# Kernel tuning notes

Hardware: AMD Instinct MI355X
Metric: run time of the kernel (lower is better)

The kernel has to match this reference:

```python
import jax, jax.numpy as jnp
import numpy as np

N_NODES = 20000
N_EDGES = 320000
N_GRAPHS = 512
N_FEAT = 29
DIMS = [N_FEAT, 1024, 512, 256, 512, 1024]
EPS = 1e-5


def setup_inputs() -> dict:
    key = jax.random.key(0)
    ks = jax.random.split(key, 32)
    inp = {}
    inp["x"] = jax.random.normal(ks[0], (N_NODES, N_FEAT), dtype=jnp.float32)
    inp["edge_index"] = jax.random.randint(ks[1], (2, N_EDGES), 0, N_NODES, dtype=jnp.int64)
    inp["batch"] = jnp.sort(jax.random.randint(ks[2], (N_NODES,), 0, N_GRAPHS, dtype=jnp.int64))
    # 5 GCNConv layers: weight [in, out] + bias, plus BN gamma/beta
    for i in range(5):
        din, dout = DIMS[i], DIMS[i + 1]
        inp[f"W{i+1}"] = jax.random.normal(ks[3 + i], (din, dout), dtype=jnp.float32) * (1.0 / np.sqrt(din))
        inp[f"b{i+1}"] = jnp.zeros((dout,), dtype=jnp.float32)
        inp[f"g{i+1}"] = jnp.ones((dout,), dtype=jnp.float32)
        inp[f"be{i+1}"] = jnp.zeros((dout,), dtype=jnp.float32)
    # attention gate Linear(1024, 1)
    inp["Wg"] = jax.random.normal(ks[10], (1024, 1), dtype=jnp.float32) * 0.03
    inp["bg"] = jnp.zeros((1,), dtype=jnp.float32)
    # MLP head
    inp["Wf2"] = jax.random.normal(ks[11], (1024, 128), dtype=jnp.float32) * 0.03
    inp["bf2"] = jnp.zeros((128,), dtype=jnp.float32)
    inp["Wf3"] = jax.random.normal(ks[12], (128, 16), dtype=jnp.float32) * 0.25
    inp["bf3"] = jnp.zeros((16,), dtype=jnp.float32)
    inp["Wf4"] = jax.random.normal(ks[13], (16, 1), dtype=jnp.float32) * 0.25
    inp["bf4"] = jnp.zeros((1,), dtype=jnp.float32)
    return inp


def _gcn_conv(x, row, col, W, b):
    # PyG GCNConv: linear transform, then D^{-1/2}(A+I)D^{-1/2} aggregation, then bias.
    n = x.shape[0]
    xw = x @ W  # [N, dout]
    deg = jax.ops.segment_sum(jnp.ones_like(col, dtype=xw.dtype), col, num_segments=n)
    dinv = jnp.where(deg > 0, jax.lax.rsqrt(deg), 0.0)
    norm = dinv[row] * dinv[col]  # [E+N]
    out = jax.ops.segment_sum(xw[row] * norm[:, None], col, num_segments=n)
    return out + b


def _bn_train(x, gamma, beta):
    m = jnp.mean(x, axis=0)
    v = jnp.var(x, axis=0)  # biased, matches torch training normalization
    return gamma * (x - m) * jax.lax.rsqrt(v + EPS) + beta


def _global_attention(x, batch, Wg, bg, n_graphs):
    gate = (x @ Wg + bg)[:, 0]  # [N]
    gmax = jax.ops.segment_max(gate, batch, num_segments=n_graphs)
    e = jnp.exp(gate - gmax[batch])
    s = jax.ops.segment_sum(e, batch, num_segments=n_graphs)
    alpha = e / s[batch]
    return jax.ops.segment_sum(alpha[:, None] * x, batch, num_segments=n_graphs)


def reference(x, edge_index, batch,
              W1, b1, g1, be1, W2, b2, g2, be2, W3, b3, g3, be3,
              W4, b4, g4, be4, W5, b5, g5, be5,
              Wg, bg, Wf2, bf2, Wf3, bf3, Wf4, bf4):
    n = x.shape[0]
    sl = jnp.arange(n, dtype=edge_index.dtype)
    row = jnp.concatenate([edge_index[0], sl])  # with self-loops
    col = jnp.concatenate([edge_index[1], sl])
    h = x
    params = [(W1, b1, g1, be1), (W2, b2, g2, be2), (W3, b3, g3, be3),
              (W4, b4, g4, be4), (W5, b5, g5, be5)]
    for (W, b, g, be) in params:
        h = jax.nn.relu(_gcn_conv(h, row, col, W, b))
        h = _bn_train(h, g, be)
    p = _global_attention(h, batch, Wg, bg, N_GRAPHS)  # [G, 1024]
    p = jax.nn.relu(p @ Wf2 + bf2)
    p = jax.nn.relu(p @ Wf3 + bf3)
    return p @ Wf4 + bf4  # [G, 1]
```

## Files before the change

### kernel.cpp

```cpp
#include <hip/hip_runtime.h>

#define EPS_BN 1e-5f

constexpr int NN   = 20000;
constexpr int NE   = 320000;
constexpr int NTOT = NE + NN;
constexpr int NG   = 512;
constexpr int MPAD = 20480;
constexpr int NBLK = 79;

typedef _Float16 half8  __attribute__((ext_vector_type(8)));
typedef _Float16 half2v __attribute__((ext_vector_type(2)));
typedef float floatx4   __attribute__((ext_vector_type(4)));

__global__ void k_deg(const int* __restrict__ col, int* __restrict__ deg,
                      const int* __restrict__ batch, int* __restrict__ gcnt) {
  int e = blockIdx.x * blockDim.x + threadIdx.x;
  if (e >= NTOT) return;
  int c = (e < NE) ? col[e] : (e - NE);
  atomicAdd(&deg[c], 1);
  if (e < NN) atomicAdd(&gcnt[batch[e]], 1);
}

__global__ __launch_bounds__(256) void k_pre1(const int* __restrict__ deg,
                                              float* __restrict__ dinvv,
                                              int* __restrict__ psum) {
  __shared__ int ws[4];
  int t = threadIdx.x, lane = t & 63, wv = t >> 6;
  int idx = blockIdx.x * 256 + t;
  int d = (idx < NN) ? deg[idx] : 0;
  if (idx < NN) dinvv[idx] = rsqrtf((float)d);
  int s = d;
  for (int o = 1; o < 64; o <<= 1) { int u = __shfl_up(s, o, 64); if (lane >= o) s += u; }
  if (lane == 63) ws[wv] = s;
  __syncthreads();
  if (t == 0) psum[blockIdx.x] = ws[0] + ws[1] + ws[2] + ws[3];
}

__global__ __launch_bounds__(256) void k_pre2(const int* __restrict__ psum,
                                              int* __restrict__ pbase,
                                              const int* __restrict__ gcnt,
                                              int* __restrict__ goff) {
  __shared__ int ws[8];
  int t = threadIdx.x, lane = t & 63, wv = t >> 6;
  int v = (t < NBLK) ? psum[t] : 0;
  int inc = v;
  for (int o = 1; o < 64; o <<= 1) { int u = __shfl_up(inc, o, 64); if (lane >= o) inc += u; }
  if (lane == 63) ws[wv] = inc;
  __syncthreads();
  int base = 0;
  for (int w = 0; w < wv; ++w) base += ws[w];
  int excl = base + inc - v;
  if (t < NBLK) pbase[t] = excl;
  if (t == NBLK - 1) pbase[NBLK] = excl + v;
  __syncthreads();
  int a0 = gcnt[2 * t], a1 = gcnt[2 * t + 1];
  int p = a0 + a1;
  int incp = p;
  for (int o = 1; o < 64; o <<= 1) { int u = __shfl_up(incp, o, 64); if (lane >= o) incp += u; }
  if (lane == 63) ws[4 + wv] = incp;
  __syncthreads();
  int gb = 0;
  for (int w = 0; w < wv; ++w) gb += ws[4 + w];
  int exclp = gb + incp - p;
  goff[2 * t]     = exclp;
  goff[2 * t + 1] = exclp + a0;
  if (t == 255) goff[NG] = exclp + p;
}

__global__ __launch_bounds__(256) void k_pre3(const int* __restrict__ deg,
                                              const int* __restrict__ pbase,
                                              int* __restrict__ indptr,
                                              int* __restrict__ cursor) {
  __shared__ int ws[4];
  int t = threadIdx.x, lane = t & 63, wv = t >> 6;
  int idx = blockIdx.x * 256 + t;
  int d = (idx < NN) ? deg[idx] : 0;
  int inc = d;
  for (int o = 1; o < 64; o <<= 1) { int u = __shfl_up(inc, o, 64); if (lane >= o) inc += u; }
  if (lane == 63) ws[wv] = inc;
  __syncthreads();
  int base = pbase[blockIdx.x];
  for (int w = 0; w < wv; ++w) base += ws[w];
  int excl = base + inc - d;
  if (idx < NN) { indptr[idx] = excl; cursor[idx] = excl; }
  if (idx == NN - 1) indptr[NN] = excl + d;
}

__global__ void k_fill(const int* __restrict__ row, const int* __restrict__ col,
                       const float* __restrict__ dinv, int* __restrict__ cursor,
                       int2* __restrict__ csw, float* __restrict__ rsum) {
  int e = blockIdx.x * blockDim.x + threadIdx.x;
  if (e >= NTOT) return;
  int r, c;
  if (e < NE) { r = row[e]; c = col[e]; } else { r = c = e - NE; }
  float wv = dinv[r] * dinv[c];
  int pos = atomicAdd(&cursor[c], 1);
  int2 m; m.x = r; m.y = __builtin_bit_cast(int, wv);
  csw[pos] = m;
  atomicAdd(&rsum[c], wv);
}

__device__ __forceinline__ size_t fragoff(int n, int k, int kb) {
  return ((size_t)(n >> 4) * kb + (k >> 5)) * 512 + ((k >> 3) & 3) * 128 + (n & 15) * 8;
}

__global__ void k_wconv3(const float* __restrict__ W0, const float* __restrict__ W3,
                         const float* __restrict__ W4,
                         _Float16* __restrict__ T0, _Float16* __restrict__ T3,
                         _Float16* __restrict__ T4) {
  int c = blockIdx.x * blockDim.x + threadIdx.x;
  _Float16 ov[8];
  if (c < 4096) {
    int n = c >> 2, k = (c & 3) * 8;
    #pragma unroll
    for (int i = 0; i < 8; ++i)
      ov[i] = (_Float16)((k + i < 29) ? W0[(size_t)(k + i) * 1024 + n] : 0.f);
    *(uint4*)&T0[fragoff(n, k, 1)] = *(const uint4*)ov;
  } else if (c < 4096 + 16384) {
    int c2 = c - 4096;
    int n = c2 >> 5, k = (c2 & 31) * 8;
    #pragma unroll
    for (int i = 0; i < 8; ++i)
      ov[i] = (_Float16)W3[(size_t)(k + i) * 512 + n];
    *(uint4*)&T3[fragoff(n, k, 8)] = *(const uint4*)ov;
  } else if (c < 4096 + 16384 + 65536) {
    int c3 = c - 20480;
    int n = c3 >> 6, k = (c3 & 63) * 8;
    #pragma unroll
    for (int i = 0; i < 8; ++i)
      ov[i] = (_Float16)W4[(size_t)(k + i) * 1024 + n];
    *(uint4*)&T4[fragoff(n, k, 16)] = *(const uint4*)ov;
  }
}

__global__ __launch_bounds__(256) void k_wfold(const float* __restrict__ W, int K, int N,
                                               const float* __restrict__ sums,
                                               const float* __restrict__ gamma,
                                               const float* __restrict__ beta,
                                               _Float16* __restrict__ T,
                                               float* __restrict__ c) {
  __shared__ float red[256];
  int n = blockIdx.x, tid = threadIdx.x;
  int kb = K >> 5;
  const float inv_n = 1.f / NN;
  float csum = 0.f;
  for (int kc = tid; kc < (K >> 3); kc += 256) {
    int k = kc * 8;
    _Float16 ov[8];
    #pragma unroll
    for (int i = 0; i < 8; ++i) {
      int ki = k + i;
      float mean = sums[ki] * inv_n;
      float var  = sums[K + ki] * inv_n - mean * mean;
      float sc   = gamma[ki] * rsqrtf(var + EPS_BN);
      float sh   = beta[ki] - mean * sc;
      float wv   = W[(size_t)ki * N + n];
      ov[i] = (_Float16)(sc * wv);
      csum += sh * wv;
    }
    *(uint4*)&T[fragoff(n, k, kb)] = *(const uint4*)ov;
  }
  red[tid] = csum;
  __syncthreads();
  for (int o = 128; o > 0; o >>= 1) {
    if (tid < o) red[tid] += red[tid + o];
    __syncthreads();
  }
  if (tid == 0) c[n] = red[0];
}

#define AGG_CH 128
__global__ __launch_bounds__(128) void k_agg29(
    const float* __restrict__ X,
    const int* __restrict__ indptr, const int2* __restrict__ csw,
    _Float16* __restrict__ Y) {
  __shared__ int   s_src[AGG_CH];
  __shared__ float s_w[AGG_CH];
  __shared__ float red[128];
  int node = blockIdx.x;
  int tid  = threadIdx.x;
  int sub  = tid / 29;
  int feat = tid - sub * 29;
  bool act = tid < 116;
  int beg = indptr[node], end = indptr[node + 1];
  float acc = 0.f;
  for (int e0 = beg; e0 < end; e0 += AGG_CH) {
    int c = min(AGG_CH, end - e0);
    if (tid < c) {
      int2 m = csw[e0 + tid];
      s_src[tid] = m.x;
      s_w[tid]   = __builtin_bit_cast(float, m.y);
    }
    __syncthreads();
    if (act) {
      for (int j = 0; j < c; j += 4) {
        int jj = j + sub;
        if (jj < c) acc += s_w[jj] * X[(size_t)s_src[jj] * 29 + feat];
      }
    }
    __syncthreads();
  }
  red[tid] = acc;
  __syncthreads();
  if (tid < 32) {
    float v = 0.f;
    if (tid < 29) v = red[tid] + red[29 + tid] + red[58 + tid] + red[87 + tid];
    size_t fb = (size_t)(node >> 4) * 512 + (size_t)(tid >> 3) * 128 + (node & 15) * 8 + (tid & 7);
    Y[fb] = (_Float16)v;
  }
}

template<int MODE>
__global__ __launch_bounds__(256) void k_aggv(
    const _Float16* __restrict__ X,
    _Float16* __restrict__ Yf, _Float16* __restrict__ Yrow,
    const int* __restrict__ indptr, const int2* __restrict__ csw,
    const float* __restrict__ rowsum,
    const float* __restrict__ p0, const float* __restrict__ p1,
    const float* __restrict__ p2)
{
  constexpr int F = 512;
  int wave = threadIdx.x >> 6;
  int lane = threadIdx.x & 63;
  int node = blockIdx.x * 4 + wave;
  int beg = indptr[node], end = indptr[node + 1];
  float acc[8];
  #pragma unroll
  for (int i = 0; i < 8; ++i) acc[i] = 0.f;
  const unsigned* Xl = (const unsigned*)X + lane * 4;

  auto body = [&](int e) {
    int2 m = csw[e];
    float we = __builtin_bit_cast(float, m.y);
    uint4 d = *(const uint4*)(Xl + (size_t)m.x * (F / 2));
    unsigned uu[4] = {d.x, d.y, d.z, d.w};
    #pragma unroll
    for (int i = 0; i < 4; ++i) {
      half2v h = __builtin_bit_cast(half2v, uu[i]);
      acc[2 * i]     = fmaf(we, (float)h[0], acc[2 * i]);
      acc[2 * i + 1] = fmaf(we, (float)h[1], acc[2 * i + 1]);
    }
  };
  int e = beg;
  for (; e + 8 <= end; e += 8) {
    body(e); body(e + 1); body(e + 2); body(e + 3);
    body(e + 4); body(e + 5); body(e + 6); body(e + 7);
  }
  for (; e < end; ++e) body(e);

  float s_n = rowsum[node];
  _Float16 outv[8];
  #pragma unroll
  for (int i = 0; i < 8; ++i) {
    int f = lane * 8 + i;
    float v;
    if constexpr (MODE == 0) {
      v = fmaxf(acc[i] + s_n * p0[f] + p1[f], 0.f);
    } else {
      const float inv_n = 1.f / NN;
      float mean = p0[f] * inv_n;
      float var  = p0[F + f] * inv_n - mean * mean;
      float sc   = p1[f] * rsqrtf(var + EPS_BN);
      float sh   = p2[f] - mean * sc;
      v = sc * acc[i] + s_n * sh;
    }
    outv[i] = (_Float16)v;
  }
  if (Yf) {
    size_t fb = (size_t)(node >> 4) * (16 * 512) + lane * 128 + (node & 15) * 8;
    *(uint4*)(Yf + fb) = *(const uint4*)outv;
  }
  if (Yrow) {
    *(uint4*)(Yrow + (size_t)node * F + lane * 8) = *(const uint4*)outv;
  }
}

template<int MODE>
__global__ __launch_bounds__(256) void k_aggp(
    const _Float16* __restrict__ X,
    _Float16* __restrict__ Yf, _Float16* __restrict__ Yrow,
    const int* __restrict__ indptr, const int2* __restrict__ csw,
    const float* __restrict__ rowsum,
    const float* __restrict__ p0, const float* __restrict__ p1,
    const float* __restrict__ p2)
{
  constexpr int F = 256;
  int wave = threadIdx.x >> 6;
  int lane = threadIdx.x & 63;
  int half = lane >> 5;
  int l32  = lane & 31;
  int node = blockIdx.x * 8 + wave * 2 + half;
  int beg = indptr[node], end = indptr[node + 1];
  int len = end - beg;
  int len0 = __shfl(len, 0, 64);
  int len1 = __shfl(len, 32, 64);
  int maxlen = max(len0, len1);

  float acc[8];
  #pragma unroll
  for (int i = 0; i < 8; ++i) acc[i] = 0.f;
  const unsigned* Xl = (const unsigned*)X + l32 * 4;

  auto body = [&](int t) {
    int e = beg + min(t, len - 1);
    int2 m = csw[e];
    float we = (t < len) ? __builtin_bit_cast(float, m.y) : 0.f;
    uint4 d = *(const uint4*)(Xl + (size_t)m.x * (F / 2));
    unsigned uu[4] = {d.x, d.y, d.z, d.w};
    #pragma unroll
    for (int i = 0; i < 4; ++i) {
      half2v h = __builtin_bit_cast(half2v, uu[i]);
      acc[2 * i]     = fmaf(we, (float)h[0], acc[2 * i]);
      acc[2 * i + 1] = fmaf(we, (float)h[1], acc[2 * i + 1]);
    }
  };
  int t = 0;
  for (; t + 4 <= maxlen; t += 4) { body(t); body(t + 1); body(t + 2); body(t + 3); }
  for (; t < maxlen; ++t) body(t);

  float s_n = rowsum[node];
  _Float16 outv[8];
  #pragma unroll
  for (int i = 0; i < 8; ++i) {
    int f = l32 * 8 + i;
    float v;
    if constexpr (MODE == 0) {
      v = fmaxf(acc[i] + s_n * p0[f] + p1[f], 0.f);
    } else {
      const float inv_n = 1.f / NN;
      float mean = p0[f] * inv_n;
      float var  = p0[F + f] * inv_n - mean * mean;
      float sc   = p1[f] * rsqrtf(var + EPS_BN);
      float sh   = p2[f] - mean * sc;
      v = sc * acc[i] + s_n * sh;
    }
    outv[i] = (_Float16)v;
  }
  if (Yf) {
    size_t fb = (size_t)(node >> 4) * (8 * 512) + l32 * 128 + (node & 15) * 8;
    *(uint4*)(Yf + fb) = *(const uint4*)outv;
  }
  if (Yrow) {
    *(uint4*)(Yrow + (size_t)node * F + l32 * 8) = *(const uint4*)outv;
  }
}

template<int K, int FRAGOUT>
__global__ __launch_bounds__(256) void k_gemmf(
    const _Float16* __restrict__ Af, const _Float16* __restrict__ Bf,
    const float* __restrict__ bias,
    _Float16* __restrict__ Ch,
    _Float16* __restrict__ Cf,
    float* __restrict__ stats,
    int N, int do_relu, int nbx)
{
  __shared__ __align__(16) _Float16 cs[128 * 136];
  __shared__ float sred[256];

  const int tid  = threadIdx.x;
  const int wave = tid >> 6;
  const int lane = tid & 63;

  int lin = blockIdx.x;
  int xcd = lin & 7, seq = lin >> 3;
  int bx = seq % nbx, grp = seq / nbx;
  int by = xcd + 8 * grp;
  const int row0 = by * 128;
  const int col0 = bx * 128;

  const int q  = lane >> 4;
  const int mm = lane & 15;
  const int wm = wave >> 1;
  const int wn = wave & 1;

  sred[tid] = 0.f;

  constexpr int KB = K / 32;
  const _Float16* pa[4];
  const _Float16* pb[4];
  #pragma unroll
  for (int i = 0; i < 4; ++i)
    pa[i] = Af + (size_t)((row0 >> 4) + wm * 4 + i) * (KB * 512) + lane * 8;
  #pragma unroll
  for (int j = 0; j < 4; ++j)
    pb[j] = Bf + (size_t)((col0 >> 4) + wn * 4 + j) * (KB * 512) + lane * 8;

  floatx4 acc[4][4];
  #pragma unroll
  for (int i = 0; i < 4; ++i)
    #pragma unroll
    for (int j = 0; j < 4; ++j) acc[i][j] = floatx4{0.f, 0.f, 0.f, 0.f};

  half8 av[4], bv[4];
  #pragma unroll
  for (int i = 0; i < 4; ++i) { av[i] = *(const half8*)pa[i]; pa[i] += 512; }
  #pragma unroll
  for (int j = 0; j < 4; ++j) { bv[j] = *(const half8*)pb[j]; pb[j] += 512; }

  #pragma unroll 2
  for (int s = 0; s < KB; ++s) {
    half8 nav[4], nbv[4];
    if (s + 1 < KB) {
      #pragma unroll
      for (int i = 0; i < 4; ++i) { nav[i] = *(const half8*)pa[i]; pa[i] += 512; }
      #pragma unroll
      for (int j = 0; j < 4; ++j) { nbv[j] = *(const half8*)pb[j]; pb[j] += 512; }
    }
    #pragma unroll
    for (int j = 0; j < 4; ++j)
      #pragma unroll
      for (int i = 0; i < 4; ++i)
        acc[i][j] = __builtin_amdgcn_mfma_f32_16x16x32_f16(av[i], bv[j], acc[i][j], 0, 0, 0);
    if (s + 1 < KB) {
      #pragma unroll
      for (int i = 0; i < 4; ++i) av[i] = nav[i];
      #pragma unroll
      for (int j = 0; j < 4; ++j) bv[j] = nbv[j];
    }
  }

  __syncthreads();

  float sloc[4]  = {0.f, 0.f, 0.f, 0.f};
  float s2loc[4] = {0.f, 0.f, 0.f, 0.f};
  #pragma unroll
  for (int j = 0; j < 4; ++j) {
    int cl = wn * 64 + j * 16 + mm;
    float bvv = bias ? bias[col0 + cl] : 0.f;
    #pragma unroll
    for (int i = 0; i < 4; ++i) {
      #pragma unroll
      for (int r = 0; r < 4; ++r) {
        int rl = wm * 64 + i * 16 + q * 4 + r;
        float v = acc[i][j][r] + bvv;
        if (do_relu) v = fmaxf(v, 0.f);
        cs[rl * 136 + cl] = (_Float16)v;
        if (row0 + rl < NN) { sloc[j] += v; s2loc[j] += v * v; }
      }
    }
  }

  if (stats) {
    #pragma unroll
    for (int j = 0; j < 4; ++j) {
      float a = sloc[j], b2 = s2loc[j];
      a  += __shfl_xor(a, 16, 64);  a  += __shfl_xor(a, 32, 64);
      b2 += __shfl_xor(b2, 16, 64); b2 += __shfl_xor(b2, 32, 64);
      if (q == 0) {
        int cl = wn * 64 + j * 16 + mm;
        atomicAdd(&sred[cl], a);
        atomicAdd(&sred[128 + cl], b2);
      }
    }
  }
  __syncthreads();

  if (FRAGOUT) {
    int mlo = tid & 15, sub = (tid >> 4) & 3, kcr = (tid >> 6) & 3;
    int kbN = N >> 5;
    #pragma unroll
    for (int pass = 0; pass < 8; ++pass) {
      int m = pass * 16 + mlo;
      int kl = kcr * 32 + sub * 8;
      uint4 d = *(const uint4*)&cs[m * 136 + kl];
      size_t fa = ((size_t)((row0 >> 4) + pass) * kbN + (col0 >> 5) + kcr) * 512
                + sub * 128 + mlo * 8;
      *(uint4*)&Cf[fa] = d;
    }
  } else {
    #pragma unroll
    for (int pass = 0; pass < 8; ++pass) {
      int cidx = tid + pass * 256;
      int r = cidx >> 4, kc = cidx & 15;
      int rr = row0 + r;
      if (rr < NN) {
        uint4 d = *(const uint4*)&cs[r * 136 + kc * 8];
        *(uint4*)&Ch[(size_t)rr * N + col0 + kc * 8] = d;
      }
    }
  }

  if (stats && tid < 128) {
    atomicAdd(&stats[col0 + tid], sred[tid]);
    atomicAdd(&stats[N + col0 + tid], sred[128 + tid]);
  }
}

template<int F>
__global__ __launch_bounds__(256) void k_statsf(const _Float16* __restrict__ Xf,
                                                float* __restrict__ sums) {
  constexpr int KB = F / 32;
  constexpr int NT = NN / 16;
  int wid  = (blockIdx.x * 256 + threadIdx.x) >> 6;
  int lane = threadIdx.x & 63;
  int nw   = (gridDim.x * 256) >> 6;
  int kidx = wid % KB;
  int ng0  = wid / KB;
  int step = nw / KB;
  int sub = lane >> 4, n16 = lane & 15;

  float s[8], s2[8];
  #pragma unroll
  for (int i = 0; i < 8; ++i) { s[i] = 0.f; s2[i] = 0.f; }

  for (int ng = ng0; ng < NT; ng += step) {
    const _Float16* p = Xf + ((size_t)ng * KB + kidx) * 512 + lane * 8;
    uint4 d = *(const uint4*)p;
    unsigned uu[4] = {d.x, d.y, d.z, d.w};
    #pragma unroll
    for (int i = 0; i < 4; ++i) {
      half2v h = __builtin_bit_cast(half2v, uu[i]);
      float v0 = (float)h[0], v1 = (float)h[1];
      s[2 * i]      += v0;  s2[2 * i]     += v0 * v0;
      s[2 * i + 1]  += v1;  s2[2 * i + 1] += v1 * v1;
    }
  }
  #pragma unroll
  for (int o = 1; o < 16; o <<= 1) {
    #pragma unroll
    for (int i = 0; i < 8; ++i) {
      s[i]  += __shfl_xor(s[i],  o, 64);
      s2[i] += __shfl_xor(s2[i], o, 64);
    }
  }
  if (n16 == 0) {
    int f = kidx * 32 + sub * 8;
    #pragma unroll
    for (int i = 0; i < 8; ++i) {
      atomicAdd(&sums[f + i], s[i]);
      atomicAdd(&sums[F + f + i], s2[i]);
    }
  }
}

__global__ __launch_bounds__(256) void k_stats16(const _Float16* __restrict__ X, int F,
                                                 float* __restrict__ sums) {
  int tid = threadIdx.x;
  int npf = F >> 8;
  float s[2] = {0.f, 0.f}, s2[2] = {0.f, 0.f};
  for (int r = blockIdx.x; r < NN; r += gridDim.x) {
    #pragma unroll
    for (int i = 0; i < 2; ++i) {
      if (i < npf) {
        float v = (float)X[(size_t)r * F + tid + i * 256];
        s[i] += v; s2[i] += v * v;
      }
    }
  }
  #pragma unroll
  for (int i = 0; i < 2; ++i) {
    if (i < npf) {
      atomicAdd(&sums[tid + i * 256], s[i]);
      atomicAdd(&sums[F + tid + i * 256], s2[i]);
    }
  }
}

__global__ __launch_bounds__(256) void k_gfold(const float* __restrict__ sums,
                                               const float* __restrict__ g5,
                                               const float* __restrict__ be5,
                                               const float* __restrict__ Wg,
                                               const float* __restrict__ bg,
                                               float* __restrict__ wgf,
                                               float* __restrict__ cg) {
  __shared__ float red[256];
  int tid = threadIdx.x;
  const float inv_n = 1.f / NN;
  float t = 0.f;
  #pragma unroll
  for (int i = 0; i < 4; ++i) {
    int f = i * 256 + tid;
    float mean = sums[f] * inv_n;
    float var  = sums[1024 + f] * inv_n - mean * mean;
    float sc   = g5[f] * rsqrtf(var + EPS_BN);
    float sh   = be5[f] - mean * sc;
    float wv   = Wg[f];
    wgf[f] = sc * wv;
    t += sh * wv;
  }
  red[tid] = t;
  __syncthreads();
  for (int o = 128; o > 0; o >>= 1) {
    if (tid < o) red[tid] += red[tid + o];
    __syncthreads();
  }
  if (tid == 0) cg[0] = red[0] + bg[0];
}

__global__ __launch_bounds__(256) void k_gate3(const _Float16* __restrict__ X,
                                               const float* __restrict__ wgf,
                                               const float* __restrict__ cg,
                                               float* __restrict__ gate) {
  int wave = threadIdx.x >> 6, lane = threadIdx.x & 63;
  int node = blockIdx.x * 4 + wave;
  const _Float16* xp = X + (size_t)node * 1024 + lane * 16;
  uint4 d0 = *(const uint4*)xp;
  uint4 d1 = *(const uint4*)(xp + 8);
  const float4* wp = (const float4*)(wgf + lane * 16);
  float4 w0 = wp[0], w1 = wp[1], w2 = wp[2], w3 = wp[3];
  float wv[16] = {w0.x, w0.y, w0.z, w0.w, w1.x, w1.y, w1.z, w1.w,
                  w2.x, w2.y, w2.z, w2.w, w3.x, w3.y, w3.z, w3.w};
  unsigned uu[8] = {d0.x, d0.y, d0.z, d0.w, d1.x, d1.y, d1.z, d1.w};
  float s = 0.f;
  #pragma unroll
  for (int i = 0; i < 8; ++i) {
    half2v h = __builtin_bit_cast(half2v, uu[i]);
    s = fmaf((float)h[0], wv[2 * i],     s);
    s = fmaf((float)h[1], wv[2 * i + 1], s);
  }
  #pragma unroll
  for (int o = 1; o < 64; o <<= 1) s += __shfl_xor(s, o, 64);
  if (lane == 0) gate[node] = s + cg[0];
}

__global__ __launch_bounds__(256) void k_poolhead(
    const _Float16* __restrict__ X, const float* __restrict__ gate,
    const int* __restrict__ goff,
    const float* __restrict__ sums, const float* __restrict__ g5,
    const float* __restrict__ be5,
    const float* __restrict__ Wf2, const float* __restrict__ bf2,
    const float* __restrict__ Wf3, const float* __restrict__ bf3,
    const float* __restrict__ Wf4, const float* __restrict__ bf4,
    float* __restrict__ out)
{
  __shared__ float red[256];
  __shared__ float sp[1024];
  __shared__ float sp2[128];
  __shared__ float sp3[16];
  int g = blockIdx.x, tid = threadIdx.x;
  int beg = goff[g], end = goff[g + 1];
  bool nonempty = end > beg;

  float m = -3.4e38f;
  for (int n = beg + tid; n < end; n += 256) m = fmaxf(m, gate[n]);
  red[tid] = m;
  __syncthreads();
  for (int o = 128; o > 0; o >>= 1) {
    if (tid < o) red[tid] = fmaxf(red[tid], red[tid + o]);
    __syncthreads();
  }
  m = red[0];
  __syncthreads();
  float s = 0.f;
  for (int n = beg + tid; n < end; n += 256) s += expf(gate[n] - m);
  red[tid] = s;
  __syncthreads();
  for (int o = 128; o > 0; o >>= 1) {
    if (tid < o) red[tid] += red[tid + o];
    __syncthreads();
  }
  float inv = nonempty ? (1.f / red[0]) : 0.f;

  int f = tid * 4;
  const float inv_n = 1.f / NN;
  float acc[4] = {0.f, 0.f, 0.f, 0.f};
  if (nonempty) {
    const _Float16* Xf = X + f;
    int n = beg;
    for (; n + 4 <= end; n += 4) {
      float a0 = expf(gate[n]     - m);
      float a1 = expf(gate[n + 1] - m);
      float a2 = expf(gate[n + 2] - m);
      float a3 = expf(gate[n + 3] - m);
      uint2 u0 = *(const uint2*)(Xf + (size_t)(n)     * 1024);
      uint2 u1 = *(const uint2*)(Xf + (size_t)(n + 1) * 1024);
      uint2 u2 = *(const uint2*)(Xf + (size_t)(n + 2) * 1024);
      uint2 u3 = *(const uint2*)(Xf + (size_t)(n + 3) * 1024);
      half2v p00 = __builtin_bit_cast(half2v, u0.x), p01 = __builtin_bit_cast(half2v, u0.y);
      half2v p10 = __builtin_bit_cast(half2v, u1.x), p11 = __builtin_bit_cast(half2v, u1.y);
      half2v p20 = __builtin_bit_cast(half2v, u2.x), p21 = __builtin_bit_cast(half2v, u2.y);
      half2v p30 = __builtin_bit_cast(half2v, u3.x), p31 = __builtin_bit_cast(half2v, u3.y);
      acc[0] += a0 * (float)p00[0] + a1 * (float)p10[0] + a2 * (float)p20[0] + a3 * (float)p30[0];
      acc[1] += a0 * (float)p00[1] + a1 * (float)p10[1] + a2 * (float)p20[1] + a3 * (float)p30[1];
      acc[2] += a0 * (float)p01[0] + a1 * (float)p11[0] + a2 * (float)p21[0] + a3 * (float)p31[0];
      acc[3] += a0 * (float)p01[1] + a1 * (float)p11[1] + a2 * (float)p21[1] + a3 * (float)p31[1];
    }
    for (; n < end; ++n) {
      float a = expf(gate[n] - m);
      uint2 u0 = *(const uint2*)(Xf + (size_t)n * 1024);
      half2v p0 = __builtin_bit_cast(half2v, u0.x), p1 = __builtin_bit_cast(half2v, u0.y);
      acc[0] += a * (float)p0[0];
      acc[1] += a * (float)p0[1];
      acc[2] += a * (float)p1[0];
      acc[3] += a * (float)p1[1];
    }
  }
  #pragma unroll
  for (int i = 0; i < 4; ++i) {
    int ff = f + i;
    float mean = sums[ff] * inv_n;
    float var  = sums[1024 + ff] * inv_n - mean * mean;
    float sc   = g5[ff] * rsqrtf(var + EPS_BN);
    float sh   = be5[ff] - mean * sc;
    sp[ff] = nonempty ? (acc[i] * inv * sc + sh) : 0.f;
  }
  __syncthreads();

  {
    int o = tid & 127, hf = tid >> 7;
    float s2 = 0.f;
    const float* wp = Wf2 + o;
    for (int k = hf * 512; k < hf * 512 + 512; ++k) s2 += sp[k] * wp[(size_t)k * 128];
    red[tid] = s2;
  }
  __syncthreads();
  if (tid < 128) sp2[tid] = fmaxf(red[tid] + red[tid + 128] + bf2[tid], 0.f);
  __syncthreads();
  if (tid < 16) {
    float t = bf3[tid];
    for (int k = 0; k < 128; ++k) t += sp2[k] * Wf3[k * 16 + tid];
    sp3[tid] = fmaxf(t, 0.f);
  }
  __syncthreads();
  if (tid == 0) {
    float t = bf4[0];
    for (int k = 0; k < 16; ++k) t += sp3[k] * Wf4[k];
    out[g] = t;
  }
}

extern "C" void kernel_launch(void* const* d_in, const int* in_sizes, int n_in,
                              void* d_out, int out_size, void* d_ws, size_t ws_size,
                              hipStream_t stream) {
  const float* x     = (const float*)d_in[0];
  const int*   ei    = (const int*)d_in[1];
  const int*   batch = (const int*)d_in[2];
  const float* W[5]; const float* b[5]; const float* g[5]; const float* be[5];
  for (int l = 0; l < 5; ++l) {
    W[l]  = (const float*)d_in[3 + 4 * l];
    b[l]  = (const float*)d_in[4 + 4 * l];
    g[l]  = (const float*)d_in[5 + 4 * l];
    be[l] = (const float*)d_in[6 + 4 * l];
  }
  const float* Wg  = (const float*)d_in[23];
  const float* bg  = (const float*)d_in[24];
  const float* Wf2 = (const float*)d_in[25];
  const float* bf2 = (const float*)d_in[26];
  const float* Wf3 = (const float*)d_in[27];
  const float* bf3 = (const float*)d_in[28];
  const float* Wf4 = (const float*)d_in[29];
  const float* bf4 = (const float*)d_in[30];
  float* out = (float*)d_out;

  const int* row = ei;
  const int* col = ei + NE;

  char* base = (char*)d_ws;
  size_t off = 0;
  auto alloc = [&](size_t bytes) -> char* {
    char* p = base + off;
    off = (off + bytes + 255) & ~(size_t)255;
    return p;
  };
  _Float16*  AH  = (_Float16*)alloc((size_t)MPAD * 1024 * 2);
  _Float16*  AF  = (_Float16*)alloc((size_t)MPAD * 512 * 2);
  _Float16*  ASM = (_Float16*)alloc((size_t)MPAD * 32 * 2);
  _Float16*  BF  = (_Float16*)alloc((size_t)NN * 512 * 2);
  _Float16*  BF2 = (_Float16*)alloc((size_t)NN * 512 * 2);
  _Float16*  H5  = (_Float16*)alloc((size_t)NN * 1024 * 2);
  const int wtsz[5] = {1024 * 32, 512 * 1024, 256 * 512, 512 * 256, 1024 * 512};
  _Float16* WT[5];
  for (int l = 0; l < 5; ++l) WT[l] = (_Float16*)alloc((size_t)wtsz[l] * 2);
  float* c2  = (float*)alloc(512 * 4);
  float* c3  = (float*)alloc(256 * 4);
  float* dinv    = (float*)alloc(NN * 4);
  int*   indptr  = (int*)alloc((NN + 1) * 4);
  int*   cursor  = (int*)alloc(NN * 4);
  int2*  csw     = (int2*)alloc((size_t)NTOT * 8);
  int*   psum    = (int*)alloc((NBLK + 1) * 4);
  int*   pbase   = (int*)alloc((NBLK + 1) * 4);
  int*   goff    = (int*)alloc((NG + 1) * 4);
  float* gate    = (float*)alloc(NN * 4);
  float* wgf     = (float*)alloc(1024 * 4);
  float* cg      = (float*)alloc(4);
  size_t znf = 6656 + NN + NG + NN;
  float* zbase = (float*)alloc(znf * 4);
  float* bns  = zbase;
  int*   deg  = (int*)(zbase + 6656);
  int*   gcnt = (int*)(zbase + 6656 + NN);
  float* rsum = zbase + 6656 + NN + NG;
  float* bns1 = bns;
  float* bns2 = bns + 2048;
  float* bns3 = bns + 3072;
  float* bns4 = bns + 3584;
  float* bns5 = bns + 4608;

  hipMemsetAsync(zbase, 0, znf * 4, stream);
  k_deg<<<(NTOT + 255) / 256, 256, 0, stream>>>(col, deg, batch, gcnt);
  k_pre1<<<NBLK, 256, 0, stream>>>(deg, dinv, psum);
  k_pre2<<<1, 256, 0, stream>>>(psum, pbase, gcnt, goff);
  k_pre3<<<NBLK, 256, 0, stream>>>(deg, pbase, indptr, cursor);
  k_fill<<<(NTOT + 255) / 256, 256, 0, stream>>>(row, col, dinv, cursor, csw, rsum);
  k_wconv3<<<336, 256, 0, stream>>>(W[0], W[3], W[4], WT[0], WT[3], WT[4]);

  k_agg29<<<NN, 128, 0, stream>>>(x, indptr, csw, ASM);
  k_gemmf<32, 1><<<8 * 160, 256, 0, stream>>>(ASM, WT[0], b[0], nullptr, AH, bns1, 1024, 1, 8);

  k_wfold<<<512, 256, 0, stream>>>(W[1], 1024, 512, bns1, g[0], be[0], WT[1], c2);
  k_gemmf<1024, 0><<<4 * 160, 256, 0, stream>>>(AH, WT[1], nullptr, BF, nullptr, nullptr, 512, 0, 4);
  k_aggv<0><<<NN / 4, 256, 0, stream>>>(BF, AF, nullptr, indptr, csw, rsum, c2, b[1], nullptr);
  k_statsf<512><<<256, 256, 0, stream>>>(AF, bns2);

  k_wfold<<<256, 256, 0, stream>>>(W[2], 512, 256, bns2, g[1], be[1], WT[2], c3);
  k_gemmf<512, 0><<<2 * 160, 256, 0, stream>>>(AF, WT[2], nullptr, BF2, nullptr, nullptr, 256, 0, 2);
  k_aggp<0><<<NN / 8, 256, 0, stream>>>(BF2, nullptr, BF, indptr, csw, rsum, c3, b[2], nullptr);
  k_stats16<<<512, 256, 0, stream>>>(BF, 256, bns3);

  k_aggp<1><<<NN / 8, 256, 0, stream>>>(BF, AH, nullptr, indptr, csw, rsum, bns3, g[2], be[2]);
  k_gemmf<256, 0><<<4 * 160, 256, 0, stream>>>(AH, WT[3], b[3], BF2, nullptr, bns4, 512, 1, 4);

  k_aggv<1><<<NN / 4, 256, 0, stream>>>(BF2, AF, nullptr, indptr, csw, rsum, bns4, g[3], be[3]);
  k_gemmf<512, 0><<<8 * 160, 256, 0, stream>>>(AF, WT[4], b[4], H5, nullptr, bns5, 1024, 1, 8);

  k_gfold<<<1, 256, 0, stream>>>(bns5, g[4], be[4], Wg, bg, wgf, cg);
  k_gate3<<<NN / 4, 256, 0, stream>>>(H5, wgf, cg, gate);
  k_poolhead<<<NG, 256, 0, stream>>>(H5, gate, goff, bns5, g[4], be[4],
                                     Wf2, bf2, Wf3, bf3, Wf4, bf4, out);
}
```

Before: 682.0 us.

## Split pooled attention head into softmax, pooling, and MLP kernels

Replaces the single per-graph pooling+head kernel with three kernels. The first computes the softmax weights once per graph with wave shuffles. The second pools with four blocks per graph over feature chunks for more parallelism. The third runs the MLP head using a transposed Wf2 so each thread reads its weight row contiguously with float4 loads. This adds two extra launches, a weight transpose kernel and a pooled intermediate buffer round-trip through global memory. Pooling loads shrink from 8-byte to 2-byte per-thread reads.

```diff
diff --git a/kernel.cpp b/kernel.cpp
--- a/kernel.cpp
+++ b/kernel.cpp
@@ -614,94 +614,86 @@
   if (lane == 0) gate[node] = s + cg[0];
 }
 
-__global__ __launch_bounds__(256) void k_poolhead(
-    const _Float16* __restrict__ X, const float* __restrict__ gate,
+__global__ __launch_bounds__(64) void k_galpha(const int* __restrict__ goff,
+                                               float* __restrict__ gate) {
+  int g = blockIdx.x, lane = threadIdx.x;
+  int beg = goff[g], end = goff[g + 1];
+  float m = -3.4e38f;
+  for (int n = beg + lane; n < end; n += 64) m = fmaxf(m, gate[n]);
+  #pragma unroll
+  for (int o = 1; o < 64; o <<= 1) m = fmaxf(m, __shfl_xor(m, o, 64));
+  float s = 0.f;
+  for (int n = beg + lane; n < end; n += 64) s += expf(gate[n] - m);
+  #pragma unroll
+  for (int o = 1; o < 64; o <<= 1) s += __shfl_xor(s, o, 64);
+  float inv = (end > beg) ? (1.f / s) : 0.f;
+  for (int n = beg + lane; n < end; n += 64) gate[n] = expf(gate[n] - m) * inv;
+}
+
+__global__ __launch_bounds__(256) void k_pool(
+    const _Float16* __restrict__ X, const float* __restrict__ alpha,
     const int* __restrict__ goff,
     const float* __restrict__ sums, const float* __restrict__ g5,
     const float* __restrict__ be5,
-    const float* __restrict__ Wf2, const float* __restrict__ bf2,
+    float* __restrict__ pooled)
+{
+  int g = blockIdx.x >> 2, fc = blockIdx.x & 3;
+  int f = fc * 256 + threadIdx.x;
+  int beg = goff[g], end = goff[g + 1];
+  const _Float16* Xp = X + f;
+  float acc = 0.f;
+  int n = beg;
+  for (; n + 4 <= end; n += 4) {
+    float a0 = alpha[n], a1 = alpha[n + 1], a2 = alpha[n + 2], a3 = alpha[n + 3];
+    float x0 = (float)Xp[(size_t)(n)     * 1024];
+    float x1 = (float)Xp[(size_t)(n + 1) * 1024];
+    float x2 = (float)Xp[(size_t)(n + 2) * 1024];
+    float x3 = (float)Xp[(size_t)(n + 3) * 1024];
+    acc += a0 * x0 + a1 * x1 + a2 * x2 + a3 * x3;
+  }
+  for (; n < end; ++n) acc += alpha[n] * (float)Xp[(size_t)n * 1024];
+
+  const float inv_n = 1.f / NN;
+  float mean = sums[f] * inv_n;
+  float var  = sums[1024 + f] * inv_n - mean * mean;
+  float sc   = g5[f] * rsqrtf(var + EPS_BN);
+  float sh   = be5[f] - mean * sc;
+  pooled[(size_t)g * 1024 + f] = (end > beg) ? (acc * sc + sh) : 0.f;
+}
+
+__global__ __launch_bounds__(256) void k_wt2(const float* __restrict__ Wf2,
+                                             float* __restrict__ Wf2T) {
+  int idx = blockIdx.x * 256 + threadIdx.x;
+  int o = idx & 127, k = idx >> 7;
+  Wf2T[(size_t)o * 1024 + k] = Wf2[idx];
+}
+
+__global__ __launch_bounds__(256) void k_head(
+    const float* __restrict__ pooled,
+    const float* __restrict__ Wf2T, const float* __restrict__ bf2,
     const float* __restrict__ Wf3, const float* __restrict__ bf3,
     const float* __restrict__ Wf4, const float* __restrict__ bf4,
     float* __restrict__ out)
 {
+  __shared__ float sp[1024];
   __shared__ float red[256];
-  __shared__ float sp[1024];
   __shared__ float sp2[128];
   __shared__ float sp3[16];
   int g = blockIdx.x, tid = threadIdx.x;
-  int beg = goff[g], end = goff[g + 1];
-  bool nonempty = end > beg;
-
-  float m = -3.4e38f;
-  for (int n = beg + tid; n < end; n += 256) m = fmaxf(m, gate[n]);
-  red[tid] = m;
-  __syncthreads();
-  for (int o = 128; o > 0; o >>= 1) {
-    if (tid < o) red[tid] = fmaxf(red[tid], red[tid + o]);
-    __syncthreads();
-  }
-  m = red[0];
-  __syncthreads();
-  float s = 0.f;
-  for (int n = beg + tid; n < end; n += 256) s += expf(gate[n] - m);
-  red[tid] = s;
-  __syncthreads();
-  for (int o = 128; o > 0; o >>= 1) {
-    if (tid < o) red[tid] += red[tid + o];
-    __syncthreads();
-  }
-  float inv = nonempty ? (1.f / red[0]) : 0.f;
-
-  int f = tid * 4;
-  const float inv_n = 1.f / NN;
-  float acc[4] = {0.f, 0.f, 0.f, 0.f};
-  if (nonempty) {
-    const _Float16* Xf = X + f;
-    int n = beg;
-    for (; n + 4 <= end; n += 4) {
-      float a0 = expf(gate[n]     - m);
-      float a1 = expf(gate[n + 1] - m);
-      float a2 = expf(gate[n + 2] - m);
-      float a3 = expf(gate[n + 3] - m);
-      uint2 u0 = *(const uint2*)(Xf + (size_t)(n)     * 1024);
-      uint2 u1 = *(const uint2*)(Xf + (size_t)(n + 1) * 1024);
-      uint2 u2 = *(const uint2*)(Xf + (size_t)(n + 2) * 1024);
-      uint2 u3 = *(const uint2*)(Xf + (size_t)(n + 3) * 1024);
-      half2v p00 = __builtin_bit_cast(half2v, u0.x), p01 = __builtin_bit_cast(half2v, u0.y);
-      half2v p10 = __builtin_bit_cast(half2v, u1.x), p11 = __builtin_bit_cast(half2v, u1.y);
-      half2v p20 = __builtin_bit_cast(half2v, u2.x), p21 = __builtin_bit_cast(half2v, u2.y);
-      half2v p30 = __builtin_bit_cast(half2v, u3.x), p31 = __builtin_bit_cast(half2v, u3.y);
-      acc[0] += a0 * (float)p00[0] + a1 * (float)p10[0] + a2 * (float)p20[0] + a3 * (float)p30[0];
-      acc[1] += a0 * (float)p00[1] + a1 * (float)p10[1] + a2 * (float)p20[1] + a3 * (float)p30[1];
-      acc[2] += a0 * (float)p01[0] + a1 * (float)p11[0] + a2 * (float)p21[0] + a3 * (float)p31[0];
-      acc[3] += a0 * (float)p01[1] + a1 * (float)p11[1] + a2 * (float)p21[1] + a3 * (float)p31[1];
-    }
-    for (; n < end; ++n) {
-      float a = expf(gate[n] - m);
-      uint2 u0 = *(const uint2*)(Xf + (size_t)n * 1024);
-      half2v p0 = __builtin_bit_cast(half2v, u0.x), p1 = __builtin_bit_cast(half2v, u0.y);
-      acc[0] += a * (float)p0[0];
-      acc[1] += a * (float)p0[1];
-      acc[2] += a * (float)p1[0];
-      acc[3] += a * (float)p1[1];
-    }
-  }
-  #pragma unroll
-  for (int i = 0; i < 4; ++i) {
-    int ff = f + i;
-    float mean = sums[ff] * inv_n;
-    float var  = sums[1024 + ff] * inv_n - mean * mean;
-    float sc   = g5[ff] * rsqrtf(var + EPS_BN);
-    float sh   = be5[ff] - mean * sc;
-    sp[ff] = nonempty ? (acc[i] * inv * sc + sh) : 0.f;
-  }
+  *(float4*)&sp[tid * 4] = *(const float4*)&pooled[(size_t)g * 1024 + tid * 4];
   __syncthreads();
 
   {
     int o = tid & 127, hf = tid >> 7;
+    const float4* wrow = (const float4*)(Wf2T + (size_t)o * 1024 + hf * 512);
+    const float* spp = &sp[hf * 512];
     float s2 = 0.f;
-    const float* wp = Wf2 + o;
-    for (int k = hf * 512; k < hf * 512 + 512; ++k) s2 += sp[k] * wp[(size_t)k * 128];
+    #pragma unroll 4
+    for (int k4 = 0; k4 < 128; ++k4) {
+      float4 w = wrow[k4];
+      s2 += w.x * spp[k4 * 4] + w.y * spp[k4 * 4 + 1]
+          + w.z * spp[k4 * 4 + 2] + w.w * spp[k4 * 4 + 3];
+    }
     red[tid] = s2;
   }
   __syncthreads();
@@ -774,6 +766,8 @@
   float* gate    = (float*)alloc(NN * 4);
   float* wgf     = (float*)alloc(1024 * 4);
   float* cg      = (float*)alloc(4);
+  float* pooled  = (float*)alloc((size_t)NG * 1024 * 4);
+  float* Wf2T    = (float*)alloc((size_t)128 * 1024 * 4);
   size_t znf = 6656 + NN + NG + NN;
   float* zbase = (float*)alloc(znf * 4);
   float* bns  = zbase;
@@ -793,6 +787,7 @@
   k_pre3<<<NBLK, 256, 0, stream>>>(deg, pbase, indptr, cursor);
   k_fill<<<(NTOT + 255) / 256, 256, 0, stream>>>(row, col, dinv, cursor, csw, rsum);
   k_wconv3<<<336, 256, 0, stream>>>(W[0], W[3], W[4], WT[0], WT[3], WT[4]);
+  k_wt2<<<512, 256, 0, stream>>>(Wf2, Wf2T);
 
   k_agg29<<<NN, 128, 0, stream>>>(x, indptr, csw, ASM);
   k_gemmf<32, 1><<<8 * 160, 256, 0, stream>>>(ASM, WT[0], b[0], nullptr, AH, bns1, 1024, 1, 8);
@@ -815,6 +810,7 @@
 
   k_gfold<<<1, 256, 0, stream>>>(bns5, g[4], be[4], Wg, bg, wgf, cg);
   k_gate3<<<NN / 4, 256, 0, stream>>>(H5, wgf, cg, gate);
-  k_poolhead<<<NG, 256, 0, stream>>>(H5, gate, goff, bns5, g[4], be[4],
-                                     Wf2, bf2, Wf3, bf3, Wf4, bf4, out);
-}
+  k_galpha<<<NG, 64, 0, stream>>>(goff, gate);
+  k_pool<<<NG * 4, 256, 0, stream>>>(H5, gate, goff, bns5, g[4], be[4], pooled);
+  k_head<<<NG, 256, 0, stream>>>(pooled, Wf2T, bf2, Wf3, bf3, Wf4, bf4, out);
+}
```

New measurement: 597.5 us. 12.4% less time.
